# Optimization experiments

Hardware: AMD Instinct MI355X
Metric: run time of the kernel (lower is better)

Reference implementation:

```python
import jax, jax.numpy as jnp
import numpy as np

D_FEATURE = 512
D_K = 512
B, LQ, N = 64, 128, 2048
NEG_BIAS = 1e10


def setup_inputs() -> dict:
    key = jax.random.key(0)
    k1, k2, k3, k4, k5, k6 = jax.random.split(key, 6)
    # xavier_uniform bound for Linear(d_feature -> d_k), weight shape [d_k, d_feature]
    bound = float(np.sqrt(6.0 / (D_FEATURE + D_K)))
    metal_feature = jax.random.normal(k1, (B, LQ, D_FEATURE), dtype=jnp.float32)
    x = jax.random.normal(k2, (B, N, D_FEATURE), dtype=jnp.float32)
    mask = jax.random.randint(k3, (B, N), 0, 2, dtype=jnp.int32)
    W_q = jax.random.uniform(k4, (D_K, D_FEATURE), jnp.float32, -bound, bound)
    W_k = jax.random.uniform(k5, (D_K, D_FEATURE), jnp.float32, -bound, bound)
    W_v = jax.random.uniform(k6, (D_K, D_FEATURE), jnp.float32, -bound, bound)
    return {"metal_feature": metal_feature, "x": x, "mask": mask,
            "W_q": W_q, "W_k": W_k, "W_v": W_v}


def reference(metal_feature, x, mask, W_q, W_k, W_v):
    # Q: [B, Lq, d_k], K/V: [B, N, d_k]  (torch Linear: y = x @ W.T, no bias)
    Q = jnp.einsum('blf,kf->blk', metal_feature, W_q)
    K = jnp.einsum('bnf,kf->bnk', x, W_k)
    V = jnp.einsum('bnf,kf->bnk', x, W_v)
    scale = 1.0 / jnp.sqrt(jnp.float32(D_K))
    # scores: [B, Lq, N] with additive mask bias (mask broadcast over queries)
    scores = jnp.einsum('blk,bnk->bln', Q, K) * scale
    scores = scores - (1.0 - mask[:, None, :].astype(scores.dtype)) * NEG_BIAS
    attn = jax.nn.softmax(scores, axis=-1)
    out = jnp.einsum('bln,bnk->blk', attn, V)
    # relu; squeeze(1) is a no-op for Lq>1; dropout identity at eval
    return jax.nn.relu(out)
```

## Files before the change

### kernel.cpp

```cpp
#include <hip/hip_runtime.h>

typedef __attribute__((ext_vector_type(4))) float   f32x4;
typedef __attribute__((ext_vector_type(8))) __bf16  bf16x8;
typedef unsigned short u16;
typedef __attribute__((ext_vector_type(8))) unsigned short u16x8;
typedef __attribute__((ext_vector_type(4))) unsigned short u16x4;

__device__ __forceinline__ u16 f2bf(float f) {
  unsigned u = __builtin_bit_cast(unsigned, f);
  u += 0x7fffu + ((u >> 16) & 1u);
  return (u16)(u >> 16);
}
__device__ __forceinline__ float bf2f(u16 h) {
  unsigned u = ((unsigned)h) << 16;
  return __builtin_bit_cast(float, u);
}
__device__ __forceinline__ void gld16(const void* g, void* l) {
  __builtin_amdgcn_global_load_lds(
      (const __attribute__((address_space(1))) void*)g,
      (__attribute__((address_space(3))) void*)l, 16, 0, 0);
}


#define SYNC_MID do { __builtin_amdgcn_sched_barrier(0); __builtin_amdgcn_s_barrier(); \
  asm volatile("s_waitcnt lgkmcnt(0)" ::: "memory"); __builtin_amdgcn_sched_barrier(0); } while(0)
#define SYNC_END do { __builtin_amdgcn_sched_barrier(0); __builtin_amdgcn_s_barrier(); \
  __builtin_amdgcn_sched_barrier(0); } while(0)
#define VM4 asm volatile("s_waitcnt vmcnt(4)" ::: "memory")
#define VM0 asm volatile("s_waitcnt vmcnt(0)" ::: "memory")

#define LDA(AQ, S, I0) \
  _Pragma("unroll") for (int f = 0; f < 2; ++f) \
  _Pragma("unroll") for (int s = 0; s < 2; ++s) { \
    const int rl = ((I0)+f)*16 + lr; \
    AQ[f*2+s] = *(const u16x8*)&SM[((S)*2 + wr)*8192 + rl*64 + (((s*4+lc) ^ (rl&7))*8)]; }

#define LDB(S) \
  _Pragma("unroll") for (int j = 0; j < 4; ++j) \
  _Pragma("unroll") for (int s = 0; s < 2; ++s) { \
    const int rl = (wc&1)*64 + j*16 + lr; \
    bq[j][s] = *(const u16x8*)&SM[32768 + ((S)*2 + (wc>>1))*8192 + rl*64 + (((s*4+lc) ^ (rl&7))*8)]; }

#define MM(AQ, I0) do { __builtin_amdgcn_s_setprio(1); \
  _Pragma("unroll") for (int f = 0; f < 2; ++f) \
  _Pragma("unroll") for (int j = 0; j < 4; ++j) \
  _Pragma("unroll") for (int s = 0; s < 2; ++s) \
    acc[(I0)+f][j] = __builtin_amdgcn_mfma_f32_16x16x32_bf16( \
      __builtin_bit_cast(bf16x8, AQ[f*2+s]), __builtin_bit_cast(bf16x8, bq[j][s]), \
      acc[(I0)+f][j], 0, 0, 0); \
  __builtin_amdgcn_s_setprio(0); } while(0)

__global__ __launch_bounds__(512, 1)
void kv8_k(const u16* __restrict__ xb, const u16* __restrict__ Wkv,
           u16* __restrict__ Kc, u16* __restrict__ Vt)
{
  __shared__ u16 SM[65536];
  const int t = threadIdx.x;
  const int w = t >> 6, lane = t & 63;
  const int wr = w >> 2, wc = w & 3;
  const int lr = lane & 15, lc = lane >> 4;

  int bx = blockIdx.x, by = blockIdx.y;
  {
    int nwg = gridDim.x * gridDim.y;
    int h = bx + 4 * by;
    int q = nwg >> 3;
    int s = (h & 7) * q + (h >> 3);
    bx = s & 3; by = s >> 2;
  }
  const int n0 = bx * 256;
  const int m0 = by * 256;
  const int KT = 8;

  f32x4 acc[8][4];
#pragma unroll
  for (int i = 0; i < 8; i++)
#pragma unroll
    for (int j = 0; j < 4; j++) acc[i][j] = f32x4{0.f, 0.f, 0.f, 0.f};
  u16x8 bq[4][2];

  auto stageA = [&](int T, int h) {
    const int S = T & 1;
#pragma unroll
    for (int r = 0; r < 2; ++r) {
      const int idx = r * 512 + w * 64;
      const int row = (idx >> 3) + (lane >> 3);
      const int slot = lane & 7;
      const u16* g = xb + (long)(m0 + h * 128 + row) * 512 + T * 64 + ((slot ^ (row & 7)) * 8);
      gld16(g, (void*)&SM[(S * 2 + h) * 8192 + idx * 8]);
    }
  };
  auto stageB = [&](int T, int h) {
    const int S = T & 1;
#pragma unroll
    for (int r = 0; r < 2; ++r) {
      const int idx = r * 512 + w * 64;
      const int row = (idx >> 3) + (lane >> 3);
      const int slot = lane & 7;
      const u16* g = Wkv + (long)(n0 + h * 128 + row) * 512 + T * 64 + ((slot ^ (row & 7)) * 8);
      gld16(g, (void*)&SM[32768 + (S * 2 + h) * 8192 + idx * 8]);
    }
  };

  stageA(0, 0); stageA(0, 1);
  stageB(0, 0); stageB(0, 1);
  stageB(1, 0); stageB(1, 1);
  VM4; __builtin_amdgcn_sched_barrier(0);
  __builtin_amdgcn_s_barrier(); __builtin_amdgcn_sched_barrier(0);

  for (int I = 0; I < KT / 2; ++I) {
    const int a = 2 * I, b = 2 * I + 1;
    const bool g2 = (a + 2) < KT;
    const bool g3 = (b + 2) < KT;
    { u16x8 aq[4]; LDB(0); LDA(aq, 0, 0); stageA(b, 0);
      SYNC_MID; MM(aq, 0); SYNC_END; }
    { u16x8 aq[4]; LDA(aq, 0, 2); stageA(b, 1);
      SYNC_MID; MM(aq, 2); SYNC_END; }
    { u16x8 aq[4]; LDA(aq, 0, 4); if (g2) stageB(a + 2, 0);
      SYNC_MID; MM(aq, 4); SYNC_END; }
    { u16x8 aq[4]; LDA(aq, 0, 6); if (g2) stageB(a + 2, 1);
      SYNC_MID; MM(aq, 6); if (g2) { VM4; } else { VM0; } SYNC_END; }
    { u16x8 aq[4]; LDB(1); LDA(aq, 1, 0); if (g2) stageA(a + 2, 0);
      SYNC_MID; MM(aq, 0); SYNC_END; }
    { u16x8 aq[4]; LDA(aq, 1, 2); if (g2) stageA(a + 2, 1);
      SYNC_MID; MM(aq, 2); SYNC_END; }
    { u16x8 aq[4]; LDA(aq, 1, 4); if (g3) stageB(b + 2, 0);
      SYNC_MID; MM(aq, 4); SYNC_END; }
    { u16x8 aq[4]; LDA(aq, 1, 6); if (g3) stageB(b + 2, 1);
      SYNC_MID; MM(aq, 6); if (g3) { VM4; } else { VM0; } SYNC_END; }
  }

#pragma unroll
  for (int i = 0; i < 8; i++) {
#pragma unroll
    for (int j = 0; j < 4; j++) {
      const int ml = wr * 128 + i * 16 + lc * 4;
      const int m  = m0 + ml;
      const int n  = n0 + wc * 64 + j * 16 + lr;
      if (n0 < 512) {
#pragma unroll
        for (int ii = 0; ii < 4; ii++)
          Kc[(long)(m + ii) * 512 + n] = f2bf(acc[i][j][ii]);
      } else {
        const int bb = m >> 11, kv = m & 2047, d = n - 512;
        u16x4 h;
#pragma unroll
        for (int ii = 0; ii < 4; ii++) h[ii] = f2bf(acc[i][j][ii]);
        *(u16x4*)(Vt + ((long)bb * 512 + d) * 2048 + kv) = h;
      }
    }
  }
}

template<int EPI>
__global__ __launch_bounds__(256)
void gemm_k(const u16* __restrict__ Ap, const u16* __restrict__ Bp,
            void* __restrict__ Cp, const int* __restrict__ maskp,
            int K, long sA, long sB, long sC, long sM, int ldc, float scale)
{
  __shared__ u16 Asb[2][4096];
  __shared__ u16 Bs [2][4096];

  const int t = threadIdx.x, z = blockIdx.z;
  const int n0 = blockIdx.x * 128, m0 = blockIdx.y * 128;
  const int KT = K / 32;
  const u16* Ab = Ap + (long)z * sA;
  const u16* Bb = Bp + (long)z * sB;

  const int w = t >> 6, lane = t & 63;
  const int m0w = (w >> 1) * 64, n0w = (w & 1) * 64;
  const int lr = lane & 15, lc = lane >> 4;

  f32x4 acc[4][4];
#pragma unroll
  for (int i = 0; i < 4; i++)
#pragma unroll
    for (int j = 0; j < 4; j++) acc[i][j] = f32x4{0.f, 0.f, 0.f, 0.f};

  auto stage = [&](int buf, int kt) {
#pragma unroll
    for (int i = 0; i < 2; i++) {
      int chunk = w * 2 + i, row = chunk * 16 + (lane >> 2), cc = lane & 3;
      const u16* g = Ab + (long)(m0 + row) * K + kt * 32 + ((cc ^ ((row >> 1) & 3)) << 3);
      gld16(g, (void*)&Asb[buf][chunk * 512]);
    }
#pragma unroll
    for (int i = 0; i < 2; i++) {
      int chunk = w * 2 + i, row = chunk * 16 + (lane >> 2), cc = lane & 3;
      const u16* g = Bb + (long)(n0 + row) * K + kt * 32 + ((cc ^ ((row >> 1) & 3)) << 3);
      gld16(g, (void*)&Bs[buf][chunk * 512]);
    }
  };
  auto compute = [&](int buf) {
    bf16x8 af[4], bv[4];
#pragma unroll
    for (int f = 0; f < 4; f++) {
      const int R = m0w + f * 16 + lr;
      af[f] = __builtin_bit_cast(bf16x8,
          *(const u16x8*)&Asb[buf][R * 32 + ((lc ^ ((R >> 1) & 3)) << 3)]);
      const int R2 = n0w + f * 16 + lr;
      bv[f] = __builtin_bit_cast(bf16x8,
          *(const u16x8*)&Bs[buf][R2 * 32 + ((lc ^ ((R2 >> 1) & 3)) << 3)]);
    }
#pragma unroll
    for (int i = 0; i < 4; i++)
#pragma unroll
      for (int j = 0; j < 4; j++)
        acc[i][j] = __builtin_amdgcn_mfma_f32_16x16x32_bf16(af[i], bv[j], acc[i][j], 0, 0, 0);
  };

  stage(0, 0);
  __syncthreads();
  int cur = 0;
  for (int kt = 1; kt < KT; ++kt) {
    stage(cur ^ 1, kt);
    compute(cur);
    __syncthreads();
    cur ^= 1;
  }
  compute(cur);

#pragma unroll
  for (int i = 0; i < 4; i++) {
#pragma unroll
    for (int j = 0; j < 4; j++) {
      const int mb = m0 + m0w + i * 16 + lc * 4;
      const int n  = n0 + n0w + j * 16 + lr;
      if constexpr (EPI == 0) {
        u16* C = (u16*)Cp + (long)z * sC;
#pragma unroll
        for (int ii = 0; ii < 4; ii++)
          C[(long)(mb + ii) * ldc + n] = f2bf(acc[i][j][ii]);
      } else if constexpr (EPI == 2) {
        const int* mk = maskp + (long)z * sM;
        u16* C = (u16*)Cp + (long)z * sC;
        const float bias = mk[n] ? 0.f : -1e10f;
#pragma unroll
        for (int ii = 0; ii < 4; ii++)
          C[(long)(mb + ii) * ldc + n] = f2bf(acc[i][j][ii] * scale + bias);
      } else {
        float* C = (float*)Cp + (long)z * sC;
#pragma unroll
        for (int ii = 0; ii < 4; ii++)
          C[(long)(mb + ii) * ldc + n] = fmaxf(acc[i][j][ii], 0.f);
      }
    }
  }
}

__global__ __launch_bounds__(256)
void wconv_k(const float* __restrict__ Wq, const float* __restrict__ Wk,
             const float* __restrict__ Wv, u16* __restrict__ Wb)
{
  long i4 = (long)blockIdx.x * 256 + threadIdx.x;
  long e  = i4 * 4;
  const float* W = (e < 262144) ? Wq : (e < 524288 ? Wk : Wv);
  long off = e & 262143;
  f32x4 f = *(const f32x4*)(W + off);
  u16x4 h;
#pragma unroll
  for (int j = 0; j < 4; j++) h[j] = f2bf(f[j]);
  *(u16x4*)(Wb + e) = h;
}

__global__ __launch_bounds__(256)
void cvt_k(const float* __restrict__ in, u16* __restrict__ out)
{
  long i = ((long)blockIdx.x * 256 + threadIdx.x) * 8;
  f32x4 a = *(const f32x4*)(in + i);
  f32x4 b = *(const f32x4*)(in + i + 4);
  u16x8 h;
#pragma unroll
  for (int j = 0; j < 4; j++) { h[j] = f2bf(a[j]); h[4 + j] = f2bf(b[j]); }
  *(u16x8*)(out + i) = h;
}

__global__ __launch_bounds__(256)
void softmax_k(u16* __restrict__ S)
{
  const long row = blockIdx.x;
  const int  t   = threadIdx.x;
  u16* R = S + row * 2048;
  u16x8 v = *(const u16x8*)(R + t * 8);
  float f[8];
#pragma unroll
  for (int j = 0; j < 8; j++) f[j] = bf2f(v[j]);
  float m = f[0];
#pragma unroll
  for (int j = 1; j < 8; j++) m = fmaxf(m, f[j]);
#pragma unroll
  for (int off = 32; off > 0; off >>= 1) m = fmaxf(m, __shfl_xor(m, off));
  __shared__ float red[4], red2[4];
  const int w = t >> 6;
  if ((t & 63) == 0) red[w] = m;
  __syncthreads();
  m = fmaxf(fmaxf(red[0], red[1]), fmaxf(red[2], red[3]));
  float e[8], s = 0.f;
#pragma unroll
  for (int j = 0; j < 8; j++) { e[j] = __expf(f[j] - m); s += e[j]; }
#pragma unroll
  for (int off = 32; off > 0; off >>= 1) s += __shfl_xor(s, off);
  if ((t & 63) == 0) red2[w] = s;
  __syncthreads();
  s = red2[0] + red2[1] + red2[2] + red2[3];
  const float inv = 1.f / s;
  u16x8 o;
#pragma unroll
  for (int j = 0; j < 8; j++) o[j] = f2bf(e[j] * inv);
  *(u16x8*)(R + t * 8) = o;
}

extern "C" void kernel_launch(void* const* d_in, const int* in_sizes, int n_in,
                              void* d_out, int out_size, void* d_ws, size_t ws_size,
                              hipStream_t stream)
{
  const float* mf   = (const float*)d_in[0];
  const float* x    = (const float*)d_in[1];
  const int*   mask = (const int*)d_in[2];
  const float* Wq   = (const float*)d_in[3];
  const float* Wk   = (const float*)d_in[4];
  const float* Wv   = (const float*)d_in[5];
  float* out = (float*)d_out;

  u16* ws  = (u16*)d_ws;
  u16* Wb  = ws;
  u16* mfb = Wb + 786432;
  u16* Qb  = mfb + 4194304;
  u16* dyn = Qb + 4194304;

  const size_t fixedB = (size_t)(786432 + 4194304 + 4194304) * 2;
  int CB = 64;
  while (CB > 1 && fixedB + (size_t)CB * 6815744ull > ws_size) CB >>= 1;

  u16* xbc = dyn;
  u16* Kc  = xbc + (size_t)CB * 1048576;
  u16* Vtc = Kc  + (size_t)CB * 1048576;
  u16* Sc  = Vtc + (size_t)CB * 1048576;

  const float scale = 0.044194173824159216f;

  wconv_k<<<768, 256, 0, stream>>>(Wq, Wk, Wv, Wb);
  cvt_k<<<2048, 256, 0, stream>>>(mf, mfb);

  gemm_k<0><<<dim3(4, 64, 1), 256, 0, stream>>>(
      mfb, Wb, Qb, nullptr, 512, 0, 0, 0, 0, 512, 1.f);

  for (int bc = 0; bc < 64; bc += CB) {
    const float* xc = x + (long)bc * 2048 * 512;
    cvt_k<<<CB * 512, 256, 0, stream>>>(xc, xbc);
    kv8_k<<<dim3(4, CB * 8, 1), 512, 0, stream>>>(xbc, Wb + 262144, Kc, Vtc);
    gemm_k<2><<<dim3(16, 1, CB), 256, 0, stream>>>(
        Qb + (long)bc * 65536, Kc, Sc, mask + (long)bc * 2048,
        512, 65536, 1048576, 262144, 2048, 2048, scale);
    softmax_k<<<CB * 128, 256, 0, stream>>>(Sc);
    gemm_k<3><<<dim3(4, 1, CB), 256, 0, stream>>>(
        Sc, Vtc, out + (long)bc * 65536, nullptr,
        2048, 262144, 1048576, 65536, 0, 512, 1.f);
  }
}
```

Baseline: 403.2 us.

## Fuse x fp32-to-bf16 conversion into KV projection GEMM with persistent batch tiles

Removes the separate cvt_k pass over x and has the K/V projection kernel load fp32 x directly, convert it to bf16 in registers and write it to LDS, with register prefetch two k-steps ahead. Each workgroup now covers a whole batch (8 M-tiles of 256 rows) for one N-tile, storing and zeroing accumulators every 8 k-steps, so the grid shrinks from CB*32 to CB*4 workgroups. This avoids writing and rereading the bf16 copy of x and frees workspace. The cost is more register pressure, synchronous loads through VGPRs instead of direct global-to-LDS copies, and fewer workgroups, which could leave compute units idle.

```diff
diff --git a/kernel.cpp b/kernel.cpp
--- a/kernel.cpp
+++ b/kernel.cpp
@@ -22,12 +22,12 @@
 }
 
 
-#define SYNC_MID do { __builtin_amdgcn_sched_barrier(0); __builtin_amdgcn_s_barrier(); \
-  asm volatile("s_waitcnt lgkmcnt(0)" ::: "memory"); __builtin_amdgcn_sched_barrier(0); } while(0)
-#define SYNC_END do { __builtin_amdgcn_sched_barrier(0); __builtin_amdgcn_s_barrier(); \
-  __builtin_amdgcn_sched_barrier(0); } while(0)
-#define VM4 asm volatile("s_waitcnt vmcnt(4)" ::: "memory")
-#define VM0 asm volatile("s_waitcnt vmcnt(0)" ::: "memory")
+#define SB __builtin_amdgcn_sched_barrier(0)
+#define SYNC_MID do { SB; __builtin_amdgcn_s_barrier(); \
+  asm volatile("s_waitcnt lgkmcnt(0)" ::: "memory"); SB; } while(0)
+#define SYNC_END do { SB; asm volatile("s_waitcnt lgkmcnt(0)" ::: "memory"); \
+  __builtin_amdgcn_s_barrier(); SB; } while(0)
+#define VM8 do { SB; asm volatile("s_waitcnt vmcnt(8)" ::: "memory"); SB; } while(0)
 
 #define LDA(AQ, S, I0) \
   _Pragma("unroll") for (int f = 0; f < 2; ++f) \
@@ -51,7 +51,7 @@
   __builtin_amdgcn_s_setprio(0); } while(0)
 
 __global__ __launch_bounds__(512, 1)
-void kv8_k(const u16* __restrict__ xb, const u16* __restrict__ Wkv,
+void kv8_k(const float* __restrict__ x, const u16* __restrict__ Wkv,
            u16* __restrict__ Kc, u16* __restrict__ Vt)
 {
   __shared__ u16 SM[65536];
@@ -59,18 +59,19 @@
   const int w = t >> 6, lane = t & 63;
   const int wr = w >> 2, wc = w & 3;
   const int lr = lane & 15, lc = lane >> 4;
+  const int ln3 = lane >> 3, sl = lane & 7;
+  const int chunk = sl ^ ln3;
 
   int bx = blockIdx.x, by = blockIdx.y;
-  {
-    int nwg = gridDim.x * gridDim.y;
-    int h = bx + 4 * by;
-    int q = nwg >> 3;
-    int s = (h & 7) * q + (h >> 3);
-    bx = s & 3; by = s >> 2;
+  if ((gridDim.y & 7) == 0) {
+    const int h = (int)(blockIdx.y * 4 + blockIdx.x);
+    const int c = h & 7, i = h >> 3;
+    const int gpc = gridDim.y >> 3;
+    bx = i / gpc;
+    by = c + (i % gpc) * 8;
   }
   const int n0 = bx * 256;
-  const int m0 = by * 256;
-  const int KT = 8;
+  const float* xg = x + (long)by * 2048 * 512;
 
   f32x4 acc[8][4];
 #pragma unroll
@@ -78,77 +79,125 @@
 #pragma unroll
     for (int j = 0; j < 4; j++) acc[i][j] = f32x4{0.f, 0.f, 0.f, 0.f};
   u16x8 bq[4][2];
-
-  auto stageA = [&](int T, int h) {
+  f32x4 preA0[4], preA1[4];
+
+  auto loadA = [&](int TT, int h, f32x4* nl) {
+    const float* g0 = xg + (long)((TT >> 3) * 256 + h * 128 + w * 8 + ln3) * 512
+                         + (TT & 7) * 64 + chunk * 8;
+    nl[0] = *(const f32x4*)g0;
+    nl[1] = *(const f32x4*)(g0 + 4);
+    nl[2] = *(const f32x4*)(g0 + 64 * 512);
+    nl[3] = *(const f32x4*)(g0 + 64 * 512 + 4);
+  };
+  auto writeA = [&](int TT, int h, f32x4* pre) {
+    u16* dst = &SM[((TT & 1) * 2 + h) * 8192];
+#pragma unroll
+    for (int r = 0; r < 2; ++r) {
+      bf16x8 v;
+#pragma unroll
+      for (int j = 0; j < 4; ++j) {
+        v[j]     = (__bf16)pre[2 * r][j];
+        v[4 + j] = (__bf16)pre[2 * r + 1][j];
+      }
+      *(u16x8*)&dst[(r * 64 + w * 8 + ln3) * 64 + sl * 8] = __builtin_bit_cast(u16x8, v);
+    }
+  };
+  auto stageB = [&](int T, int h) {
     const int S = T & 1;
 #pragma unroll
     for (int r = 0; r < 2; ++r) {
       const int idx = r * 512 + w * 64;
-      const int row = (idx >> 3) + (lane >> 3);
-      const int slot = lane & 7;
-      const u16* g = xb + (long)(m0 + h * 128 + row) * 512 + T * 64 + ((slot ^ (row & 7)) * 8);
-      gld16(g, (void*)&SM[(S * 2 + h) * 8192 + idx * 8]);
-    }
-  };
-  auto stageB = [&](int T, int h) {
-    const int S = T & 1;
-#pragma unroll
-    for (int r = 0; r < 2; ++r) {
-      const int idx = r * 512 + w * 64;
-      const int row = (idx >> 3) + (lane >> 3);
-      const int slot = lane & 7;
-      const u16* g = Wkv + (long)(n0 + h * 128 + row) * 512 + T * 64 + ((slot ^ (row & 7)) * 8);
+      const int row = (idx >> 3) + ln3;
+      const u16* g = Wkv + (long)(n0 + h * 128 + row) * 512 + (T & 7) * 64
+                         + ((sl ^ (row & 7)) * 8);
       gld16(g, (void*)&SM[32768 + (S * 2 + h) * 8192 + idx * 8]);
     }
   };
-
-  stageA(0, 0); stageA(0, 1);
-  stageB(0, 0); stageB(0, 1);
-  stageB(1, 0); stageB(1, 1);
-  VM4; __builtin_amdgcn_sched_barrier(0);
-  __builtin_amdgcn_s_barrier(); __builtin_amdgcn_sched_barrier(0);
-
-  for (int I = 0; I < KT / 2; ++I) {
+  auto epi = [&](int mt) {
+#pragma unroll
+    for (int i = 0; i < 8; i++)
+#pragma unroll
+      for (int j = 0; j < 4; j++) {
+        const int ml = mt * 256 + wr * 128 + i * 16 + lc * 4;
+        const int n  = n0 + wc * 64 + j * 16 + lr;
+        if (n0 < 512) {
+#pragma unroll
+          for (int ii = 0; ii < 4; ii++)
+            Kc[((long)by * 2048 + ml + ii) * 512 + n] = f2bf(acc[i][j][ii]);
+        } else {
+          u16x4 hh;
+#pragma unroll
+          for (int ii = 0; ii < 4; ii++) hh[ii] = f2bf(acc[i][j][ii]);
+          *(u16x4*)(Vt + ((long)by * 512 + (n - 512)) * 2048 + ml) = hh;
+        }
+        acc[i][j] = f32x4{0.f, 0.f, 0.f, 0.f};
+      }
+  };
+
+  {
+    f32x4 tp0[4], tp1[4];
+    loadA(0, 0, tp0); loadA(0, 1, tp1);
+    writeA(0, 0, tp0); writeA(0, 1, tp1);
+    loadA(1, 0, preA0); loadA(1, 1, preA1);
+    stageB(0, 0); stageB(0, 1); stageB(1, 0); stageB(1, 1);
+    asm volatile("s_waitcnt lgkmcnt(0)" ::: "memory");
+    SB; asm volatile("s_waitcnt vmcnt(4)" ::: "memory"); SB;
+    __builtin_amdgcn_s_barrier(); SB;
+  }
+
+  const int NT = 64;
+#pragma unroll 1
+  for (int I = 0; I < NT / 2; ++I) {
     const int a = 2 * I, b = 2 * I + 1;
-    const bool g2 = (a + 2) < KT;
-    const bool g3 = (b + 2) < KT;
-    { u16x8 aq[4]; LDB(0); LDA(aq, 0, 0); stageA(b, 0);
+    const bool g2 = (a + 2) < NT;
+    const bool g3 = (b + 2) < NT;
+    { f32x4 nl[4]; u16x8 aq[4];
+      if (g2) loadA(a + 2, 0, nl);
+      VM8;
+      writeA(b, 0, preA0);
+#pragma unroll
+      for (int q = 0; q < 4; ++q) preA0[q] = nl[q];
+      LDB(0); LDA(aq, 0, 0);
       SYNC_MID; MM(aq, 0); SYNC_END; }
-    { u16x8 aq[4]; LDA(aq, 0, 2); stageA(b, 1);
+    { f32x4 nl[4]; u16x8 aq[4];
+      if (g2) loadA(a + 2, 1, nl);
+      writeA(b, 1, preA1);
+#pragma unroll
+      for (int q = 0; q < 4; ++q) preA1[q] = nl[q];
+      LDA(aq, 0, 2);
       SYNC_MID; MM(aq, 2); SYNC_END; }
-    { u16x8 aq[4]; LDA(aq, 0, 4); if (g2) stageB(a + 2, 0);
+    { u16x8 aq[4];
+      if (g2) stageB(a + 2, 0);
+      LDA(aq, 0, 4);
       SYNC_MID; MM(aq, 4); SYNC_END; }
-    { u16x8 aq[4]; LDA(aq, 0, 6); if (g2) stageB(a + 2, 1);
-      SYNC_MID; MM(aq, 6); if (g2) { VM4; } else { VM0; } SYNC_END; }
-    { u16x8 aq[4]; LDB(1); LDA(aq, 1, 0); if (g2) stageA(a + 2, 0);
+    { u16x8 aq[4];
+      if (g2) stageB(a + 2, 1);
+      LDA(aq, 0, 6);
+      SYNC_MID; MM(aq, 6); SYNC_END; }
+    { f32x4 nl[4]; u16x8 aq[4];
+      if (g3) loadA(b + 2, 0, nl);
+      VM8;
+      if (g2) writeA(a + 2, 0, preA0);
+#pragma unroll
+      for (int q = 0; q < 4; ++q) preA0[q] = nl[q];
+      LDB(1); LDA(aq, 1, 0);
       SYNC_MID; MM(aq, 0); SYNC_END; }
-    { u16x8 aq[4]; LDA(aq, 1, 2); if (g2) stageA(a + 2, 1);
+    { f32x4 nl[4]; u16x8 aq[4];
+      if (g3) loadA(b + 2, 1, nl);
+      if (g2) writeA(a + 2, 1, preA1);
+#pragma unroll
+      for (int q = 0; q < 4; ++q) preA1[q] = nl[q];
+      LDA(aq, 1, 2);
       SYNC_MID; MM(aq, 2); SYNC_END; }
-    { u16x8 aq[4]; LDA(aq, 1, 4); if (g3) stageB(b + 2, 0);
+    { u16x8 aq[4];
+      if (g3) stageB(b + 2, 0);
+      LDA(aq, 1, 4);
       SYNC_MID; MM(aq, 4); SYNC_END; }
-    { u16x8 aq[4]; LDA(aq, 1, 6); if (g3) stageB(b + 2, 1);
-      SYNC_MID; MM(aq, 6); if (g3) { VM4; } else { VM0; } SYNC_END; }
-  }
-
-#pragma unroll
-  for (int i = 0; i < 8; i++) {
-#pragma unroll
-    for (int j = 0; j < 4; j++) {
-      const int ml = wr * 128 + i * 16 + lc * 4;
-      const int m  = m0 + ml;
-      const int n  = n0 + wc * 64 + j * 16 + lr;
-      if (n0 < 512) {
-#pragma unroll
-        for (int ii = 0; ii < 4; ii++)
-          Kc[(long)(m + ii) * 512 + n] = f2bf(acc[i][j][ii]);
-      } else {
-        const int bb = m >> 11, kv = m & 2047, d = n - 512;
-        u16x4 h;
-#pragma unroll
-        for (int ii = 0; ii < 4; ii++) h[ii] = f2bf(acc[i][j][ii]);
-        *(u16x4*)(Vt + ((long)bb * 512 + d) * 2048 + kv) = h;
-      }
-    }
+    { u16x8 aq[4];
+      if (g3) stageB(b + 2, 1);
+      LDA(aq, 1, 6);
+      SYNC_MID; MM(aq, 6); SYNC_END; }
+    if ((I & 3) == 3) epi(I >> 2);
   }
 }
 
@@ -330,11 +379,10 @@
 
   const size_t fixedB = (size_t)(786432 + 4194304 + 4194304) * 2;
   int CB = 64;
-  while (CB > 1 && fixedB + (size_t)CB * 6815744ull > ws_size) CB >>= 1;
-
-  u16* xbc = dyn;
-  u16* Kc  = xbc + (size_t)CB * 1048576;
-  u16* Vtc = Kc  + (size_t)CB * 1048576;
+  while (CB > 1 && fixedB + (size_t)CB * 4718592ull > ws_size) CB >>= 1;
+
+  u16* Kc  = dyn;
+  u16* Vtc = Kc + (size_t)CB * 1048576;
   u16* Sc  = Vtc + (size_t)CB * 1048576;
 
   const float scale = 0.044194173824159216f;
@@ -347,8 +395,7 @@
 
   for (int bc = 0; bc < 64; bc += CB) {
     const float* xc = x + (long)bc * 2048 * 512;
-    cvt_k<<<CB * 512, 256, 0, stream>>>(xc, xbc);
-    kv8_k<<<dim3(4, CB * 8, 1), 512, 0, stream>>>(xbc, Wb + 262144, Kc, Vtc);
+    kv8_k<<<dim3(4, CB, 1), 512, 0, stream>>>(xc, Wb + 262144, Kc, Vtc);
     gemm_k<2><<<dim3(16, 1, CB), 256, 0, stream>>>(
         Qb + (long)bc * 65536, Kc, Sc, mask + (long)bc * 2048,
         512, 65536, 1048576, 262144, 2048, 2048, scale);
```

Result: slower. 681.9 us (+69.1%).

## Make K/V projection kernel persistent per batch with 4-wave 256x256 tiles

Applied to the files above, without the earlier changes.

The K/V projection kernel now uses 256-thread blocks where each wave owns a 128x128 output sub-tile (8x8 MFMA accumulators). Each block walks all eight 256-row M-tiles of one batch in a single pipelined 64-step loop, writing each tile's epilogue as it finishes. The grid shrinks from CB*32 to CB*4 blocks and gets a new block-index swizzle intended to improve L2 locality. This cuts block launch and prologue overhead and keeps the double-buffered pipeline running across tiles. In exchange each CU has fewer waves to hide latency, register pressure is high, and the epilogue stores stall the pipeline.

```diff
diff --git a/kernel.cpp b/kernel.cpp
--- a/kernel.cpp
+++ b/kernel.cpp
@@ -21,134 +21,143 @@
       (__attribute__((address_space(3))) void*)l, 16, 0, 0);
 }
 
-
-#define SYNC_MID do { __builtin_amdgcn_sched_barrier(0); __builtin_amdgcn_s_barrier(); \
-  asm volatile("s_waitcnt lgkmcnt(0)" ::: "memory"); __builtin_amdgcn_sched_barrier(0); } while(0)
-#define SYNC_END do { __builtin_amdgcn_sched_barrier(0); __builtin_amdgcn_s_barrier(); \
-  __builtin_amdgcn_sched_barrier(0); } while(0)
-#define VM4 asm volatile("s_waitcnt vmcnt(4)" ::: "memory")
-#define VM0 asm volatile("s_waitcnt vmcnt(0)" ::: "memory")
-
-#define LDA(AQ, S, I0) \
-  _Pragma("unroll") for (int f = 0; f < 2; ++f) \
-  _Pragma("unroll") for (int s = 0; s < 2; ++s) { \
-    const int rl = ((I0)+f)*16 + lr; \
-    AQ[f*2+s] = *(const u16x8*)&SM[((S)*2 + wr)*8192 + rl*64 + (((s*4+lc) ^ (rl&7))*8)]; }
-
-#define LDB(S) \
-  _Pragma("unroll") for (int j = 0; j < 4; ++j) \
-  _Pragma("unroll") for (int s = 0; s < 2; ++s) { \
-    const int rl = (wc&1)*64 + j*16 + lr; \
-    bq[j][s] = *(const u16x8*)&SM[32768 + ((S)*2 + (wc>>1))*8192 + rl*64 + (((s*4+lc) ^ (rl&7))*8)]; }
-
-#define MM(AQ, I0) do { __builtin_amdgcn_s_setprio(1); \
-  _Pragma("unroll") for (int f = 0; f < 2; ++f) \
-  _Pragma("unroll") for (int j = 0; j < 4; ++j) \
-  _Pragma("unroll") for (int s = 0; s < 2; ++s) \
-    acc[(I0)+f][j] = __builtin_amdgcn_mfma_f32_16x16x32_bf16( \
-      __builtin_bit_cast(bf16x8, AQ[f*2+s]), __builtin_bit_cast(bf16x8, bq[j][s]), \
-      acc[(I0)+f][j], 0, 0, 0); \
-  __builtin_amdgcn_s_setprio(0); } while(0)
-
-__global__ __launch_bounds__(512, 1)
+#define SB __builtin_amdgcn_sched_barrier(0)
+#define SYNC_MID do { SB; __builtin_amdgcn_s_barrier(); \
+  asm volatile("s_waitcnt lgkmcnt(0)" ::: "memory"); SB; } while(0)
+#define SYNC_END do { SB; __builtin_amdgcn_s_barrier(); SB; } while(0)
+#define VM8 do { SB; asm volatile("s_waitcnt vmcnt(8)" ::: "memory"); SB; } while(0)
+#define VM0 do { SB; asm volatile("s_waitcnt vmcnt(0)" ::: "memory"); SB; } while(0)
+
+__global__ __launch_bounds__(256, 1)
 void kv8_k(const u16* __restrict__ xb, const u16* __restrict__ Wkv,
            u16* __restrict__ Kc, u16* __restrict__ Vt)
 {
   __shared__ u16 SM[65536];
   const int t = threadIdx.x;
   const int w = t >> 6, lane = t & 63;
-  const int wr = w >> 2, wc = w & 3;
+  const int wr = w >> 1, wc = w & 1;
   const int lr = lane & 15, lc = lane >> 4;
 
-  int bx = blockIdx.x, by = blockIdx.y;
-  {
-    int nwg = gridDim.x * gridDim.y;
-    int h = bx + 4 * by;
-    int q = nwg >> 3;
-    int s = (h & 7) * q + (h >> 3);
-    bx = s & 3; by = s >> 2;
-  }
+  int bx, by;
+  if (gridDim.y == 64) {
+    const int h = (int)(blockIdx.y * 4 + blockIdx.x);
+    const int c = h & 7, i = h >> 3;
+    by = c + (i & 7) * 8;
+    bx = i >> 3;
+  } else { bx = blockIdx.x; by = blockIdx.y; }
   const int n0 = bx * 256;
-  const int m0 = by * 256;
-  const int KT = 8;
-
-  f32x4 acc[8][4];
+  const u16* xg = xb + (long)by * 2048 * 512;
+
+  f32x4 acc[8][8];
 #pragma unroll
   for (int i = 0; i < 8; i++)
 #pragma unroll
-    for (int j = 0; j < 4; j++) acc[i][j] = f32x4{0.f, 0.f, 0.f, 0.f};
-  u16x8 bq[4][2];
-
-  auto stageA = [&](int T, int h) {
-    const int S = T & 1;
-#pragma unroll
-    for (int r = 0; r < 2; ++r) {
-      const int idx = r * 512 + w * 64;
-      const int row = (idx >> 3) + (lane >> 3);
-      const int slot = lane & 7;
-      const u16* g = xb + (long)(m0 + h * 128 + row) * 512 + T * 64 + ((slot ^ (row & 7)) * 8);
-      gld16(g, (void*)&SM[(S * 2 + h) * 8192 + idx * 8]);
-    }
-  };
-  auto stageB = [&](int T, int h) {
-    const int S = T & 1;
-#pragma unroll
-    for (int r = 0; r < 2; ++r) {
-      const int idx = r * 512 + w * 64;
-      const int row = (idx >> 3) + (lane >> 3);
-      const int slot = lane & 7;
-      const u16* g = Wkv + (long)(n0 + h * 128 + row) * 512 + T * 64 + ((slot ^ (row & 7)) * 8);
-      gld16(g, (void*)&SM[32768 + (S * 2 + h) * 8192 + idx * 8]);
-    }
+    for (int j = 0; j < 8; j++) acc[i][j] = f32x4{0.f, 0.f, 0.f, 0.f};
+  u16x8 bq[8][2];
+
+  auto stageA = [&](int TT, int h) {
+#pragma unroll
+    for (int r = 0; r < 4; ++r) {
+      const int c = r * 256 + t;
+      const int row = c >> 3, slot = c & 7;
+      const u16* g = xg + (long)((TT >> 3) * 256 + h * 128 + row) * 512
+                        + (TT & 7) * 64 + ((slot ^ (row & 7)) * 8);
+      gld16(g, (void*)&SM[((TT & 1) * 2 + h) * 8192 + c * 8]);
+    }
+  };
+  auto stageB = [&](int TT, int h) {
+#pragma unroll
+    for (int r = 0; r < 4; ++r) {
+      const int c = r * 256 + t;
+      const int row = c >> 3, slot = c & 7;
+      const u16* g = Wkv + (long)(n0 + h * 128 + row) * 512
+                         + (TT & 7) * 64 + ((slot ^ (row & 7)) * 8);
+      gld16(g, (void*)&SM[32768 + ((TT & 1) * 2 + h) * 8192 + c * 8]);
+    }
+  };
+  auto ldb = [&](int S) {
+#pragma unroll
+    for (int j = 0; j < 8; ++j)
+#pragma unroll
+      for (int s = 0; s < 2; ++s) {
+        const int rl = j * 16 + lr;
+        bq[j][s] = *(const u16x8*)&SM[32768 + (S * 2 + wc) * 8192 + rl * 64
+                                      + (((s * 4 + lc) ^ (rl & 7)) * 8)];
+      }
+  };
+  auto lda = [&](u16x8 (&aq)[2][2], int S, int I0) {
+#pragma unroll
+    for (int f = 0; f < 2; ++f)
+#pragma unroll
+      for (int s = 0; s < 2; ++s) {
+        const int rl = (I0 + f) * 16 + lr;
+        aq[f][s] = *(const u16x8*)&SM[(S * 2 + wr) * 8192 + rl * 64
+                                      + (((s * 4 + lc) ^ (rl & 7)) * 8)];
+      }
+  };
+  auto mm = [&](u16x8 (&aq)[2][2], int I0) {
+    __builtin_amdgcn_s_setprio(1);
+#pragma unroll
+    for (int f = 0; f < 2; ++f)
+#pragma unroll
+      for (int j = 0; j < 8; ++j)
+#pragma unroll
+        for (int s = 0; s < 2; ++s)
+          acc[I0 + f][j] = __builtin_amdgcn_mfma_f32_16x16x32_bf16(
+              __builtin_bit_cast(bf16x8, aq[f][s]), __builtin_bit_cast(bf16x8, bq[j][s]),
+              acc[I0 + f][j], 0, 0, 0);
+    __builtin_amdgcn_s_setprio(0);
+  };
+  auto epi = [&](int mt) {
+#pragma unroll
+    for (int i = 0; i < 8; i++)
+#pragma unroll
+      for (int j = 0; j < 8; j++) {
+        const int ml = mt * 256 + wr * 128 + i * 16 + lc * 4;
+        const int n  = n0 + wc * 128 + j * 16 + lr;
+        if (n0 < 512) {
+#pragma unroll
+          for (int ii = 0; ii < 4; ii++)
+            Kc[((long)by * 2048 + ml + ii) * 512 + n] = f2bf(acc[i][j][ii]);
+        } else {
+          u16x4 hh;
+#pragma unroll
+          for (int ii = 0; ii < 4; ii++) hh[ii] = f2bf(acc[i][j][ii]);
+          *(u16x4*)(Vt + ((long)by * 512 + (n - 512)) * 2048 + ml) = hh;
+        }
+        acc[i][j] = f32x4{0.f, 0.f, 0.f, 0.f};
+      }
   };
 
   stageA(0, 0); stageA(0, 1);
   stageB(0, 0); stageB(0, 1);
   stageB(1, 0); stageB(1, 1);
-  VM4; __builtin_amdgcn_sched_barrier(0);
-  __builtin_amdgcn_s_barrier(); __builtin_amdgcn_sched_barrier(0);
-
-  for (int I = 0; I < KT / 2; ++I) {
+  VM8;
+  __builtin_amdgcn_s_barrier(); SB;
+
+  const int NT = 64;
+#pragma unroll 1
+  for (int I = 0; I < NT / 2; ++I) {
     const int a = 2 * I, b = 2 * I + 1;
-    const bool g2 = (a + 2) < KT;
-    const bool g3 = (b + 2) < KT;
-    { u16x8 aq[4]; LDB(0); LDA(aq, 0, 0); stageA(b, 0);
-      SYNC_MID; MM(aq, 0); SYNC_END; }
-    { u16x8 aq[4]; LDA(aq, 0, 2); stageA(b, 1);
-      SYNC_MID; MM(aq, 2); SYNC_END; }
-    { u16x8 aq[4]; LDA(aq, 0, 4); if (g2) stageB(a + 2, 0);
-      SYNC_MID; MM(aq, 4); SYNC_END; }
-    { u16x8 aq[4]; LDA(aq, 0, 6); if (g2) stageB(a + 2, 1);
-      SYNC_MID; MM(aq, 6); if (g2) { VM4; } else { VM0; } SYNC_END; }
-    { u16x8 aq[4]; LDB(1); LDA(aq, 1, 0); if (g2) stageA(a + 2, 0);
-      SYNC_MID; MM(aq, 0); SYNC_END; }
-    { u16x8 aq[4]; LDA(aq, 1, 2); if (g2) stageA(a + 2, 1);
-      SYNC_MID; MM(aq, 2); SYNC_END; }
-    { u16x8 aq[4]; LDA(aq, 1, 4); if (g3) stageB(b + 2, 0);
-      SYNC_MID; MM(aq, 4); SYNC_END; }
-    { u16x8 aq[4]; LDA(aq, 1, 6); if (g3) stageB(b + 2, 1);
-      SYNC_MID; MM(aq, 6); if (g3) { VM4; } else { VM0; } SYNC_END; }
-  }
-
-#pragma unroll
-  for (int i = 0; i < 8; i++) {
-#pragma unroll
-    for (int j = 0; j < 4; j++) {
-      const int ml = wr * 128 + i * 16 + lc * 4;
-      const int m  = m0 + ml;
-      const int n  = n0 + wc * 64 + j * 16 + lr;
-      if (n0 < 512) {
-#pragma unroll
-        for (int ii = 0; ii < 4; ii++)
-          Kc[(long)(m + ii) * 512 + n] = f2bf(acc[i][j][ii]);
-      } else {
-        const int bb = m >> 11, kv = m & 2047, d = n - 512;
-        u16x4 h;
-#pragma unroll
-        for (int ii = 0; ii < 4; ii++) h[ii] = f2bf(acc[i][j][ii]);
-        *(u16x4*)(Vt + ((long)bb * 512 + d) * 2048 + kv) = h;
-      }
-    }
+    const bool g2 = (a + 2) < NT;
+    const bool g3 = (b + 2) < NT;
+    { u16x8 aq[2][2]; ldb(0); lda(aq, 0, 0); stageA(b, 0);
+      SYNC_MID; mm(aq, 0); SYNC_END; }
+    { u16x8 aq[2][2]; lda(aq, 0, 2); stageA(b, 1);
+      SYNC_MID; mm(aq, 2); SYNC_END; }
+    { u16x8 aq[2][2]; lda(aq, 0, 4); if (g2) stageB(a + 2, 0);
+      SYNC_MID; mm(aq, 4); SYNC_END; }
+    { u16x8 aq[2][2]; lda(aq, 0, 6); if (g2) stageB(a + 2, 1);
+      SYNC_MID; mm(aq, 6); if (g2) { VM8; } else { VM0; } SYNC_END; }
+    { u16x8 aq[2][2]; ldb(1); lda(aq, 1, 0); if (g2) stageA(a + 2, 0);
+      SYNC_MID; mm(aq, 0); SYNC_END; }
+    { u16x8 aq[2][2]; lda(aq, 1, 2); if (g2) stageA(a + 2, 1);
+      SYNC_MID; mm(aq, 2); SYNC_END; }
+    { u16x8 aq[2][2]; lda(aq, 1, 4); if (g3) stageB(b + 2, 0);
+      SYNC_MID; mm(aq, 4); SYNC_END; }
+    { u16x8 aq[2][2]; lda(aq, 1, 6); if (g3) stageB(b + 2, 1);
+      SYNC_MID; mm(aq, 6); if (g3) { VM8; } else { VM0; } SYNC_END; }
+    if ((I & 3) == 3) epi(I >> 2);
   }
 }
 
@@ -348,7 +357,7 @@
   for (int bc = 0; bc < 64; bc += CB) {
     const float* xc = x + (long)bc * 2048 * 512;
     cvt_k<<<CB * 512, 256, 0, stream>>>(xc, xbc);
-    kv8_k<<<dim3(4, CB * 8, 1), 512, 0, stream>>>(xbc, Wb + 262144, Kc, Vtc);
+    kv8_k<<<dim3(4, CB, 1), 256, 0, stream>>>(xbc, Wb + 262144, Kc, Vtc);
     gemm_k<2><<<dim3(16, 1, CB), 256, 0, stream>>>(
         Qb + (long)bc * 65536, Kc, Sc, mask + (long)bc * 2048,
         512, 65536, 1048576, 262144, 2048, 2048, scale);
```

Measured after the change: 1.283 ms. 218% more time.

## Make KV projection kernel persistent over a batch's rows, reusing weight tiles

Applied to the files above, without the earlier changes.

The KV projection kernel now launches one workgroup per (batch, 256-column slice) instead of one per 256x256 tile. Each workgroup loops over all eight 256-row tiles of its batch, streaming the K dimension continuously and writing the epilogue every 8 K-steps, so the pipeline prologue and drain are paid once rather than per tile. The block-to-CU swizzle is rewritten for the 64-row grid case, and the wait macros gain scheduling barriers. The grid shrinks by 8x, which may leave CUs idle when the chunk size is small, and the epilogue stores now stall the software pipeline mid-loop.

```diff
diff --git a/kernel.cpp b/kernel.cpp
--- a/kernel.cpp
+++ b/kernel.cpp
@@ -22,12 +22,12 @@
 }
 
 
-#define SYNC_MID do { __builtin_amdgcn_sched_barrier(0); __builtin_amdgcn_s_barrier(); \
-  asm volatile("s_waitcnt lgkmcnt(0)" ::: "memory"); __builtin_amdgcn_sched_barrier(0); } while(0)
-#define SYNC_END do { __builtin_amdgcn_sched_barrier(0); __builtin_amdgcn_s_barrier(); \
-  __builtin_amdgcn_sched_barrier(0); } while(0)
-#define VM4 asm volatile("s_waitcnt vmcnt(4)" ::: "memory")
-#define VM0 asm volatile("s_waitcnt vmcnt(0)" ::: "memory")
+#define SB __builtin_amdgcn_sched_barrier(0)
+#define SYNC_MID do { SB; __builtin_amdgcn_s_barrier(); \
+  asm volatile("s_waitcnt lgkmcnt(0)" ::: "memory"); SB; } while(0)
+#define SYNC_END do { SB; __builtin_amdgcn_s_barrier(); SB; } while(0)
+#define VM4 do { SB; asm volatile("s_waitcnt vmcnt(4)" ::: "memory"); SB; } while(0)
+#define VM0 do { SB; asm volatile("s_waitcnt vmcnt(0)" ::: "memory"); SB; } while(0)
 
 #define LDA(AQ, S, I0) \
   _Pragma("unroll") for (int f = 0; f < 2; ++f) \
@@ -60,17 +60,15 @@
   const int wr = w >> 2, wc = w & 3;
   const int lr = lane & 15, lc = lane >> 4;
 
-  int bx = blockIdx.x, by = blockIdx.y;
-  {
-    int nwg = gridDim.x * gridDim.y;
-    int h = bx + 4 * by;
-    int q = nwg >> 3;
-    int s = (h & 7) * q + (h >> 3);
-    bx = s & 3; by = s >> 2;
-  }
+  int bx, by;
+  if (gridDim.y == 64) {
+    const int h = (int)(blockIdx.y * 4 + blockIdx.x);
+    const int c = h & 7, i = h >> 3;
+    by = c + 8 * (i & 7);
+    bx = i >> 3;
+  } else { bx = blockIdx.x; by = blockIdx.y; }
   const int n0 = bx * 256;
-  const int m0 = by * 256;
-  const int KT = 8;
+  const u16* xg = xb + (long)by * 2048 * 512;
 
   f32x4 acc[8][4];
 #pragma unroll
@@ -79,39 +77,59 @@
     for (int j = 0; j < 4; j++) acc[i][j] = f32x4{0.f, 0.f, 0.f, 0.f};
   u16x8 bq[4][2];
 
-  auto stageA = [&](int T, int h) {
-    const int S = T & 1;
+  auto stageA = [&](int TT, int h) {
 #pragma unroll
     for (int r = 0; r < 2; ++r) {
-      const int idx = r * 512 + w * 64;
-      const int row = (idx >> 3) + (lane >> 3);
-      const int slot = lane & 7;
-      const u16* g = xb + (long)(m0 + h * 128 + row) * 512 + T * 64 + ((slot ^ (row & 7)) * 8);
-      gld16(g, (void*)&SM[(S * 2 + h) * 8192 + idx * 8]);
-    }
-  };
-  auto stageB = [&](int T, int h) {
-    const int S = T & 1;
+      const int c = r * 512 + t;
+      const int row = c >> 3, slot = c & 7;
+      const u16* g = xg + (long)((TT >> 3) * 256 + h * 128 + row) * 512
+                        + (TT & 7) * 64 + ((slot ^ (row & 7)) * 8);
+      gld16(g, (void*)&SM[((TT & 1) * 2 + h) * 8192 + c * 8]);
+    }
+  };
+  auto stageB = [&](int TT, int h) {
 #pragma unroll
     for (int r = 0; r < 2; ++r) {
-      const int idx = r * 512 + w * 64;
-      const int row = (idx >> 3) + (lane >> 3);
-      const int slot = lane & 7;
-      const u16* g = Wkv + (long)(n0 + h * 128 + row) * 512 + T * 64 + ((slot ^ (row & 7)) * 8);
-      gld16(g, (void*)&SM[32768 + (S * 2 + h) * 8192 + idx * 8]);
-    }
+      const int c = r * 512 + t;
+      const int row = c >> 3, slot = c & 7;
+      const u16* g = Wkv + (long)(n0 + h * 128 + row) * 512
+                         + (TT & 7) * 64 + ((slot ^ (row & 7)) * 8);
+      gld16(g, (void*)&SM[32768 + ((TT & 1) * 2 + h) * 8192 + c * 8]);
+    }
+  };
+  auto epi = [&](int mt) {
+#pragma unroll
+    for (int i = 0; i < 8; i++)
+#pragma unroll
+      for (int j = 0; j < 4; j++) {
+        const int ml = mt * 256 + wr * 128 + i * 16 + lc * 4;
+        const int n  = n0 + wc * 64 + j * 16 + lr;
+        if (n0 < 512) {
+#pragma unroll
+          for (int ii = 0; ii < 4; ii++)
+            Kc[((long)by * 2048 + ml + ii) * 512 + n] = f2bf(acc[i][j][ii]);
+        } else {
+          u16x4 hh;
+#pragma unroll
+          for (int ii = 0; ii < 4; ii++) hh[ii] = f2bf(acc[i][j][ii]);
+          *(u16x4*)(Vt + ((long)by * 512 + (n - 512)) * 2048 + ml) = hh;
+        }
+        acc[i][j] = f32x4{0.f, 0.f, 0.f, 0.f};
+      }
   };
 
   stageA(0, 0); stageA(0, 1);
   stageB(0, 0); stageB(0, 1);
   stageB(1, 0); stageB(1, 1);
-  VM4; __builtin_amdgcn_sched_barrier(0);
-  __builtin_amdgcn_s_barrier(); __builtin_amdgcn_sched_barrier(0);
-
-  for (int I = 0; I < KT / 2; ++I) {
+  VM4;
+  __builtin_amdgcn_s_barrier(); SB;
+
+  const int NT = 64;
+#pragma unroll 1
+  for (int I = 0; I < NT / 2; ++I) {
     const int a = 2 * I, b = 2 * I + 1;
-    const bool g2 = (a + 2) < KT;
-    const bool g3 = (b + 2) < KT;
+    const bool g2 = (a + 2) < NT;
+    const bool g3 = (b + 2) < NT;
     { u16x8 aq[4]; LDB(0); LDA(aq, 0, 0); stageA(b, 0);
       SYNC_MID; MM(aq, 0); SYNC_END; }
     { u16x8 aq[4]; LDA(aq, 0, 2); stageA(b, 1);
@@ -128,27 +146,7 @@
       SYNC_MID; MM(aq, 4); SYNC_END; }
     { u16x8 aq[4]; LDA(aq, 1, 6); if (g3) stageB(b + 2, 1);
       SYNC_MID; MM(aq, 6); if (g3) { VM4; } else { VM0; } SYNC_END; }
-  }
-
-#pragma unroll
-  for (int i = 0; i < 8; i++) {
-#pragma unroll
-    for (int j = 0; j < 4; j++) {
-      const int ml = wr * 128 + i * 16 + lc * 4;
-      const int m  = m0 + ml;
-      const int n  = n0 + wc * 64 + j * 16 + lr;
-      if (n0 < 512) {
-#pragma unroll
-        for (int ii = 0; ii < 4; ii++)
-          Kc[(long)(m + ii) * 512 + n] = f2bf(acc[i][j][ii]);
-      } else {
-        const int bb = m >> 11, kv = m & 2047, d = n - 512;
-        u16x4 h;
-#pragma unroll
-        for (int ii = 0; ii < 4; ii++) h[ii] = f2bf(acc[i][j][ii]);
-        *(u16x4*)(Vt + ((long)bb * 512 + d) * 2048 + kv) = h;
-      }
-    }
+    if ((I & 3) == 3) epi(I >> 2);
   }
 }
 
@@ -348,7 +346,7 @@
   for (int bc = 0; bc < 64; bc += CB) {
     const float* xc = x + (long)bc * 2048 * 512;
     cvt_k<<<CB * 512, 256, 0, stream>>>(xc, xbc);
-    kv8_k<<<dim3(4, CB * 8, 1), 512, 0, stream>>>(xbc, Wb + 262144, Kc, Vtc);
+    kv8_k<<<dim3(4, CB, 1), 512, 0, stream>>>(xbc, Wb + 262144, Kc, Vtc);
     gemm_k<2><<<dim3(16, 1, CB), 256, 0, stream>>>(
         Qb + (long)bc * 65536, Kc, Sc, mask + (long)bc * 2048,
         512, 65536, 1048576, 262144, 2048, 2048, scale);
```

Result: faster. 392.0 us (-2.8%).
